# Kernel tuning notes

Measured on AMD Instinct MI355X. Metric: run time of the kernel, lower is better.

The kernel has to match this reference:

```python
import jax, jax.numpy as jnp
import numpy as np
import math

H = 12          # num_attention_heads
DIM = 768       # hidden_size
HD = DIM // H   # attention_head_size
B = 8           # batch
S = 1024        # max_seqlen
NNZ = B * S     # total_nnz (all sequences full length)


def setup_inputs() -> dict:
    key = jax.random.key(0)
    k1, k2, k3, k4 = jax.random.split(key, 4)
    hidden_states = jax.random.normal(k1, (NNZ, DIM), jnp.float32)
    cu_seqlens = jnp.arange(B + 1, dtype=jnp.int32) * S
    indices = jnp.arange(NNZ, dtype=jnp.int32)
    attn_mask = jnp.ones((B, S), jnp.int32)
    bias = jax.random.normal(k2, (B, H, S, S), jnp.float32) * 0.1
    slopes = jax.random.uniform(k3, (H,), jnp.float32)
    # Wqkv = nn.Linear(DIM, 3*DIM): weight (3*DIM, DIM), bias (3*DIM,)
    Wqkv_w = jax.random.normal(k4, (3 * DIM, DIM), jnp.float32) * (1.0 / math.sqrt(DIM))
    Wqkv_b = jnp.zeros((3 * DIM,), jnp.float32)
    return {
        "hidden_states": hidden_states,
        "cu_seqlens": cu_seqlens,
        "max_seqlen": S,
        "indices": indices,
        "attn_mask": attn_mask,
        "bias": bias,
        "slopes": slopes,
        "Wqkv_w": Wqkv_w,
        "Wqkv_b": Wqkv_b,
    }


def reference(hidden_states, cu_seqlens, max_seqlen, indices, attn_mask, bias, slopes, Wqkv_w, Wqkv_b):
    nnz, dim = hidden_states.shape
    batch = cu_seqlens.shape[0] - 1
    hd = dim // H
    # fused QKV projection on unpadded tokens
    qkv = hidden_states @ Wqkv_w.T + Wqkv_b                      # (nnz, 3*dim)
    # pad_input: scatter tokens into dense (batch*seqlen, 3*dim)
    padded = jnp.zeros((batch * max_seqlen, 3 * dim), qkv.dtype).at[indices].set(qkv)
    qkv = padded.reshape(batch, max_seqlen, 3, H, hd)            # (b, s, 3, h, d)
    q, k, v = qkv[:, :, 0], qkv[:, :, 1], qkv[:, :, 2]           # (b, s, h, d)
    scores = jnp.einsum('bqhd,bkhd->bhqk', q, k) / math.sqrt(hd) + bias
    probs = jax.nn.softmax(scores, axis=-1)                      # (b, h, q, k)
    attn = jnp.einsum('bhqk,bkhd->bqhd', probs, v)               # (b, s, h, d)
    # unpad_input_only: gather valid tokens (attn_mask selects same positions as indices)
    flat = attn.reshape(batch * max_seqlen, dim)
    return flat[indices].reshape(nnz, dim)
```

## Files before the change

### kernel.cpp

```cpp
#include <hip/hip_runtime.h>

#define H_      12
#define DIM_    768
#define HD_     64
#define BATCH_  8
#define SEQ_    1024
#define NNZ_    8192
#define N3_     2304

typedef short sh8 __attribute__((ext_vector_type(8)));
typedef float f32x4 __attribute__((ext_vector_type(4)));

__device__ __forceinline__ unsigned short f2bf(float f) {
    unsigned u = __float_as_uint(f);
    u += 0x7fff + ((u >> 16) & 1);
    return (unsigned short)(u >> 16);
}

__device__ __forceinline__ void glds16(const unsigned short* g, unsigned short* l) {
    __builtin_amdgcn_global_load_lds(
        (const __attribute__((address_space(1))) unsigned int*)g,
        (__attribute__((address_space(3))) unsigned int*)l, 16, 0, 0);
}

__global__ void prep(const float* __restrict__ hidden,
                     const float* __restrict__ W,
                     const int* __restrict__ indices,
                     unsigned short* __restrict__ Xbf,
                     unsigned short* __restrict__ Wbf,
                     int* __restrict__ inv) {
    const int XN4 = NNZ_ * DIM_ / 4;
    const int WN4 = N3_ * DIM_ / 4;
    int i = blockIdx.x * blockDim.x + threadIdx.x;
    if (i < XN4) {
        float4 f = ((const float4*)hidden)[i];
        ushort4 u;
        u.x = f2bf(f.x); u.y = f2bf(f.y); u.z = f2bf(f.z); u.w = f2bf(f.w);
        ((ushort4*)Xbf)[i] = u;
    } else if (i < XN4 + WN4) {
        int k = i - XN4;
        float4 f = ((const float4*)W)[k];
        ushort4 u;
        u.x = f2bf(f.x); u.y = f2bf(f.y); u.z = f2bf(f.z); u.w = f2bf(f.w);
        ((ushort4*)Wbf)[k] = u;
    }
    if (i < NNZ_) inv[indices[i]] = i;
}

#define BK 32
__launch_bounds__(256)
__global__ void qkv_gemm(const unsigned short* __restrict__ X,
                         const unsigned short* __restrict__ W,
                         const float* __restrict__ bqkv,
                         const int* __restrict__ indices,
                         unsigned short* __restrict__ qkvbf) {
    __shared__ __align__(16) unsigned short As[128 * BK];
    __shared__ __align__(16) unsigned short Bs[128 * BK];

    const int bm = blockIdx.x * 128;
    const int bn = blockIdx.y * 128;
    const int t = threadIdx.x;
    const int wave = t >> 6;
    const int lane = t & 63;
    const int l16 = lane & 15;
    const int quad = lane >> 4;
    const int wm = (wave & 1) * 64;
    const int wn = (wave >> 1) * 64;

    f32x4 acc[4][4];
    for (int i = 0; i < 4; i++)
        for (int j = 0; j < 4; j++)
            for (int r = 0; r < 4; r++) acc[i][j][r] = 0.f;

    const int c0 = wave * 2;
    const int r0 = c0 * 16 + (lane >> 2);
    const int colA = (lane & 3) * 8;
    const unsigned short* gA0 = &X[(size_t)(bm + r0) * DIM_ + colA];
    const unsigned short* gA1 = &X[(size_t)(bm + r0 + 16) * DIM_ + colA];
    const unsigned short* gB0 = &W[(size_t)(bn + r0) * DIM_ + colA];
    const unsigned short* gB1 = &W[(size_t)(bn + r0 + 16) * DIM_ + colA];
    unsigned short* lA0 = &As[c0 * 512];
    unsigned short* lA1 = &As[c0 * 512 + 512];
    unsigned short* lB0 = &Bs[c0 * 512];
    unsigned short* lB1 = &Bs[c0 * 512 + 512];

    for (int kk = 0; kk < DIM_; kk += BK) {
        __syncthreads();
        glds16(gA0 + kk, lA0);
        glds16(gA1 + kk, lA1);
        glds16(gB0 + kk, lB0);
        glds16(gB1 + kk, lB1);
        __syncthreads();

        sh8 af[4], wf[4];
        for (int i = 0; i < 4; i++)
            af[i] = *(const sh8*)&As[(wm + i * 16 + l16) * BK + quad * 8];
        for (int j = 0; j < 4; j++)
            wf[j] = *(const sh8*)&Bs[(wn + j * 16 + l16) * BK + quad * 8];
        for (int i = 0; i < 4; i++)
            for (int j = 0; j < 4; j++)
                acc[i][j] = __builtin_amdgcn_mfma_f32_16x16x32_bf16(af[i], wf[j], acc[i][j], 0, 0, 0);
    }

    const size_t plane = (size_t)BATCH_ * H_ * SEQ_ * HD_;
    for (int i = 0; i < 4; i++) {
        for (int r = 0; r < 4; r++) {
            int m = bm + wm + i * 16 + quad * 4 + r;
            int pos = indices[m];
            int b = pos >> 10;
            int s = pos & 1023;
            for (int j = 0; j < 4; j++) {
                int n = bn + wn + j * 16 + l16;
                float val = acc[i][j][r] + bqkv[n];
                int which = n / DIM_;
                int nn = n - which * DIM_;
                int hh = nn >> 6;
                int d = nn & 63;
                size_t off;
                if (which == 2)
                    off = 2 * plane + (((size_t)b * H_ + hh) * HD_ + d) * SEQ_ + s;
                else
                    off = (size_t)which * plane + (((size_t)b * H_ + hh) * SEQ_ + s) * HD_ + d;
                qkvbf[off] = f2bf(val);
            }
        }
    }
}

#define LDP 72
__launch_bounds__(256)
__global__ void attn(const unsigned short* __restrict__ qkvbf,
                     const float* __restrict__ bias,
                     const int* __restrict__ inv,
                     float* __restrict__ out) {
    __shared__ __align__(16) unsigned short Ks2[2][64 * 32];
    __shared__ __align__(16) unsigned short Vt2[2][64 * 32];
    __shared__ __align__(16) unsigned short Ps[4][16 * LDP];

    const int qt = blockIdx.x;
    const int bh = blockIdx.y;
    const int t = threadIdx.x;
    const int wave = t >> 6;
    const int lane = t & 63;
    const int l16 = lane & 15;
    const int quad = lane >> 4;

    const size_t plane = (size_t)BATCH_ * H_ * SEQ_ * HD_;
    const unsigned short* Q  = qkvbf + (size_t)bh * SEQ_ * HD_;
    const unsigned short* K  = Q + plane;
    const unsigned short* Vt = qkvbf + 2 * plane + (size_t)bh * HD_ * SEQ_;

    const int q0 = qt * 64 + wave * 16;

    sh8 aq[2];
    for (int kk2 = 0; kk2 < 2; kk2++)
        aq[kk2] = *(const sh8*)&Q[(size_t)(q0 + l16) * HD_ + kk2 * 32 + quad * 8];

    float l_p[4] = {0.f, 0.f, 0.f, 0.f};
    f32x4 o[4];
    for (int j = 0; j < 4; j++)
        for (int r = 0; r < 4; r++) o[j][r] = 0.f;

    const float scale = 0.125f;
    const float* brow = bias + (size_t)bh * SEQ_ * SEQ_;

    const int lrow = wave * 16 + (lane >> 2);
    const int lcol = (lane & 3) * 8;
    const unsigned short* gK = &K[(size_t)lrow * HD_ + lcol];
    const unsigned short* gV = &Vt[(size_t)lrow * SEQ_ + lcol];
    unsigned short* lK0 = &Ks2[0][wave * 512];
    unsigned short* lK1 = &Ks2[1][wave * 512];
    unsigned short* lV0 = &Vt2[0][wave * 512];
    unsigned short* lV1 = &Vt2[1][wave * 512];

    for (int kt = 0; kt < 16; kt++) {
        const int k0 = kt * 64;

        float bv[4][4];
        for (int j = 0; j < 4; j++)
            for (int r = 0; r < 4; r++)
                bv[j][r] = brow[(size_t)(q0 + quad * 4 + r) * SEQ_ + k0 + j * 16 + l16];

        __syncthreads();
        glds16(gK + (size_t)k0 * HD_,      lK0);
        glds16(gK + (size_t)k0 * HD_ + 32, lK1);
        glds16(gV + k0,      lV0);
        glds16(gV + k0 + 32, lV1);
        __syncthreads();

        f32x4 sc[4];
        for (int j = 0; j < 4; j++)
            for (int r = 0; r < 4; r++) sc[j][r] = 0.f;
        for (int kk2 = 0; kk2 < 2; kk2++)
            for (int j = 0; j < 4; j++) {
                sh8 bk = *(const sh8*)&Ks2[kk2][(j * 16 + l16) * 32 + quad * 8];
                sc[j] = __builtin_amdgcn_mfma_f32_16x16x32_bf16(aq[kk2], bk, sc[j], 0, 0, 0);
            }

        for (int j = 0; j < 4; j++)
            for (int r = 0; r < 4; r++) {
                float p = __expf(sc[j][r] * scale + bv[j][r]);
                l_p[r] += p;
                Ps[wave][(quad * 4 + r) * LDP + j * 16 + l16] = f2bf(p);
            }

        for (int kk2 = 0; kk2 < 2; kk2++) {
            sh8 ap = *(const sh8*)&Ps[wave][l16 * LDP + kk2 * 32 + quad * 8];
            for (int j = 0; j < 4; j++) {
                sh8 vv = *(const sh8*)&Vt2[kk2][(j * 16 + l16) * 32 + quad * 8];
                o[j] = __builtin_amdgcn_mfma_f32_16x16x32_bf16(ap, vv, o[j], 0, 0, 0);
            }
        }
    }

    float l_i[4];
    for (int r = 0; r < 4; r++) {
        float s0 = l_p[r];
        for (int off = 1; off < 16; off <<= 1)
            s0 += __shfl_xor(s0, off, 64);
        l_i[r] = s0;
    }

    const int b = bh / H_;
    const int hh = bh % H_;
    for (int r = 0; r < 4; r++) {
        int srow_q = q0 + quad * 4 + r;
        int pos = b * SEQ_ + srow_q;
        int i_out = inv[pos];
        float rl = 1.0f / l_i[r];
        for (int j = 0; j < 4; j++)
            out[(size_t)i_out * DIM_ + hh * HD_ + j * 16 + l16] = o[j][r] * rl;
    }
}

extern "C" void kernel_launch(void* const* d_in, const int* in_sizes, int n_in,
                              void* d_out, int out_size, void* d_ws, size_t ws_size,
                              hipStream_t stream) {
    const float* hidden  = (const float*)d_in[0];
    const int*   indices = (const int*)d_in[3];
    const float* bias    = (const float*)d_in[5];
    const float* Wqkv_w  = (const float*)d_in[7];
    const float* Wqkv_b  = (const float*)d_in[8];
    float* out = (float*)d_out;

    char* ws = (char*)d_ws;
    unsigned short* Xbf   = (unsigned short*)ws;
    unsigned short* Wbf   = (unsigned short*)(ws + 12582912);
    unsigned short* qkvbf = (unsigned short*)(ws + 16121856);
    int* inv              = (int*)(ws + 53870592);

    const int XN4 = NNZ_ * DIM_ / 4;
    const int WN4 = N3_ * DIM_ / 4;
    prep<<<(XN4 + WN4 + 255) / 256, 256, 0, stream>>>(hidden, Wqkv_w, indices, Xbf, Wbf, inv);
    qkv_gemm<<<dim3(NNZ_ / 128, N3_ / 128), 256, 0, stream>>>(Xbf, Wbf, Wqkv_b, indices, qkvbf);
    attn<<<dim3(SEQ_ / 64, BATCH_ * H_), 256, 0, stream>>>(qkvbf, bias, inv, out);
}
```

Measured before the change: 639.4 us.

## Double-buffer K/V tiles, prefetch bias, swizzle LDS and transpose score MFMA

Rewrites the attention kernel's main loop to double-buffer the K and V tiles in LDS, issuing the next tile's async loads before computing on the current one and dropping one barrier per iteration. Bias is prefetched one tile ahead as float4 rows, made possible by swapping the MFMA operands so each lane holds contiguous key columns. An XOR swizzle on LDS slots is meant to reduce bank conflicts, and the block index is remapped to improve cache locality. It also sets an occupancy hint of 3 blocks per SM. Costs are a larger LDS footprint and more register pressure, which could limit occupancy.

```diff
diff --git a/kernel.cpp b/kernel.cpp
--- a/kernel.cpp
+++ b/kernel.cpp
@@ -128,22 +128,26 @@
 }
 
 #define LDP 72
-__launch_bounds__(256)
+__launch_bounds__(256, 3)
 __global__ void attn(const unsigned short* __restrict__ qkvbf,
                      const float* __restrict__ bias,
                      const int* __restrict__ inv,
                      float* __restrict__ out) {
-    __shared__ __align__(16) unsigned short Ks2[2][64 * 32];
-    __shared__ __align__(16) unsigned short Vt2[2][64 * 32];
+    __shared__ __align__(16) unsigned short Kp[2][2][64 * 32];
+    __shared__ __align__(16) unsigned short Vp[2][2][64 * 32];
     __shared__ __align__(16) unsigned short Ps[4][16 * LDP];
 
-    const int qt = blockIdx.x;
-    const int bh = blockIdx.y;
+    const int orig = blockIdx.y * gridDim.x + blockIdx.x;
+    const int swz = (orig & 7) * 192 + (orig >> 3);
+    const int qt = swz & 15;
+    const int bh = swz >> 4;
+
     const int t = threadIdx.x;
     const int wave = t >> 6;
     const int lane = t & 63;
     const int l16 = lane & 15;
     const int quad = lane >> 4;
+    const int qx = quad ^ (l16 & 3);
 
     const size_t plane = (size_t)BATCH_ * H_ * SEQ_ * HD_;
     const unsigned short* Q  = qkvbf + (size_t)bh * SEQ_ * HD_;
@@ -156,70 +160,96 @@
     for (int kk2 = 0; kk2 < 2; kk2++)
         aq[kk2] = *(const sh8*)&Q[(size_t)(q0 + l16) * HD_ + kk2 * 32 + quad * 8];
 
-    float l_p[4] = {0.f, 0.f, 0.f, 0.f};
+    float lsum = 0.f;
     f32x4 o[4];
     for (int j = 0; j < 4; j++)
         for (int r = 0; r < 4; r++) o[j][r] = 0.f;
 
     const float scale = 0.125f;
-    const float* brow = bias + (size_t)bh * SEQ_ * SEQ_;
+    const float* brow4 = bias + (size_t)bh * SEQ_ * SEQ_ + (size_t)(q0 + l16) * SEQ_ + quad * 4;
 
     const int lrow = wave * 16 + (lane >> 2);
-    const int lcol = (lane & 3) * 8;
-    const unsigned short* gK = &K[(size_t)lrow * HD_ + lcol];
-    const unsigned short* gV = &Vt[(size_t)lrow * SEQ_ + lcol];
-    unsigned short* lK0 = &Ks2[0][wave * 512];
-    unsigned short* lK1 = &Ks2[1][wave * 512];
-    unsigned short* lV0 = &Vt2[0][wave * 512];
-    unsigned short* lV1 = &Vt2[1][wave * 512];
+    const int lslot = (lane & 3) ^ ((lane >> 2) & 3);
+    const unsigned short* gK = &K[(size_t)lrow * HD_ + lslot * 8];
+    const unsigned short* gV = &Vt[(size_t)lrow * SEQ_ + lslot * 8];
+    unsigned short* lK0[2] = { &Kp[0][0][wave * 512], &Kp[0][1][wave * 512] };
+    unsigned short* lK1[2] = { &Kp[1][0][wave * 512], &Kp[1][1][wave * 512] };
+    unsigned short* lV0[2] = { &Vp[0][0][wave * 512], &Vp[0][1][wave * 512] };
+    unsigned short* lV1[2] = { &Vp[1][0][wave * 512], &Vp[1][1][wave * 512] };
+
+    glds16(gK,      lK0[0]);
+    glds16(gK + 32, lK0[1]);
+    glds16(gV,      lV0[0]);
+    glds16(gV + 32, lV0[1]);
+    float4 bv4[4];
+    for (int j = 0; j < 4; j++)
+        bv4[j] = *(const float4*)(brow4 + j * 16);
+    __syncthreads();
 
     for (int kt = 0; kt < 16; kt++) {
-        const int k0 = kt * 64;
-
-        float bv[4][4];
-        for (int j = 0; j < 4; j++)
-            for (int r = 0; r < 4; r++)
-                bv[j][r] = brow[(size_t)(q0 + quad * 4 + r) * SEQ_ + k0 + j * 16 + l16];
-
-        __syncthreads();
-        glds16(gK + (size_t)k0 * HD_,      lK0);
-        glds16(gK + (size_t)k0 * HD_ + 32, lK1);
-        glds16(gV + k0,      lV0);
-        glds16(gV + k0 + 32, lV1);
-        __syncthreads();
+        const int cur = kt & 1;
+
+        if (kt < 15) {
+            const int k0n = (kt + 1) * 64;
+            if (cur == 0) {
+                glds16(gK + (size_t)k0n * HD_,      lK1[0]);
+                glds16(gK + (size_t)k0n * HD_ + 32, lK1[1]);
+                glds16(gV + k0n,      lV1[0]);
+                glds16(gV + k0n + 32, lV1[1]);
+            } else {
+                glds16(gK + (size_t)k0n * HD_,      lK0[0]);
+                glds16(gK + (size_t)k0n * HD_ + 32, lK0[1]);
+                glds16(gV + k0n,      lV0[0]);
+                glds16(gV + k0n + 32, lV0[1]);
+            }
+        }
+        float4 bvn[4];
+        {
+            const int kb = ((kt + 1) & 15) * 64;
+            for (int j = 0; j < 4; j++)
+                bvn[j] = *(const float4*)(brow4 + kb + j * 16);
+        }
+        __builtin_amdgcn_sched_barrier(0);
 
         f32x4 sc[4];
         for (int j = 0; j < 4; j++)
             for (int r = 0; r < 4; r++) sc[j][r] = 0.f;
         for (int kk2 = 0; kk2 < 2; kk2++)
             for (int j = 0; j < 4; j++) {
-                sh8 bk = *(const sh8*)&Ks2[kk2][(j * 16 + l16) * 32 + quad * 8];
-                sc[j] = __builtin_amdgcn_mfma_f32_16x16x32_bf16(aq[kk2], bk, sc[j], 0, 0, 0);
-            }
-
-        for (int j = 0; j < 4; j++)
-            for (int r = 0; r < 4; r++) {
-                float p = __expf(sc[j][r] * scale + bv[j][r]);
-                l_p[r] += p;
-                Ps[wave][(quad * 4 + r) * LDP + j * 16 + l16] = f2bf(p);
-            }
+                sh8 bk = *(const sh8*)&Kp[cur][kk2][(j * 16 + l16) * 32 + qx * 8];
+                sc[j] = __builtin_amdgcn_mfma_f32_16x16x32_bf16(bk, aq[kk2], sc[j], 0, 0, 0);
+            }
+
+        for (int j = 0; j < 4; j++) {
+            float4 bb = bv4[j];
+            float p0 = __expf(sc[j][0] * scale + bb.x);
+            float p1 = __expf(sc[j][1] * scale + bb.y);
+            float p2 = __expf(sc[j][2] * scale + bb.z);
+            float p3 = __expf(sc[j][3] * scale + bb.w);
+            lsum += (p0 + p1) + (p2 + p3);
+            ushort4 u;
+            u.x = f2bf(p0); u.y = f2bf(p1); u.z = f2bf(p2); u.w = f2bf(p3);
+            *(ushort4*)&Ps[wave][l16 * LDP + j * 16 + quad * 4] = u;
+        }
 
         for (int kk2 = 0; kk2 < 2; kk2++) {
             sh8 ap = *(const sh8*)&Ps[wave][l16 * LDP + kk2 * 32 + quad * 8];
             for (int j = 0; j < 4; j++) {
-                sh8 vv = *(const sh8*)&Vt2[kk2][(j * 16 + l16) * 32 + quad * 8];
-                o[j] = __builtin_amdgcn_mfma_f32_16x16x32_bf16(ap, vv, o[j], 0, 0, 0);
-            }
-        }
-    }
-
-    float l_i[4];
-    for (int r = 0; r < 4; r++) {
-        float s0 = l_p[r];
-        for (int off = 1; off < 16; off <<= 1)
-            s0 += __shfl_xor(s0, off, 64);
-        l_i[r] = s0;
-    }
+                sh8 vvf = *(const sh8*)&Vp[cur][kk2][(j * 16 + l16) * 32 + qx * 8];
+                o[j] = __builtin_amdgcn_mfma_f32_16x16x32_bf16(ap, vvf, o[j], 0, 0, 0);
+            }
+        }
+
+        __syncthreads();
+        for (int j = 0; j < 4; j++) bv4[j] = bvn[j];
+    }
+
+    float s0 = lsum;
+    s0 += __shfl_xor(s0, 16, 64);
+    s0 += __shfl_xor(s0, 32, 64);
+    float rl[4];
+    for (int r = 0; r < 4; r++)
+        rl[r] = 1.0f / __shfl(s0, quad * 4 + r, 64);
 
     const int b = bh / H_;
     const int hh = bh % H_;
@@ -227,9 +257,8 @@
         int srow_q = q0 + quad * 4 + r;
         int pos = b * SEQ_ + srow_q;
         int i_out = inv[pos];
-        float rl = 1.0f / l_i[r];
-        for (int j = 0; j < 4; j++)
-            out[(size_t)i_out * DIM_ + hh * HD_ + j * 16 + l16] = o[j][r] * rl;
+        for (int j = 0; j < 4; j++)
+            out[(size_t)i_out * DIM_ + hh * HD_ + j * 16 + l16] = o[j][r] * rl[r];
     }
 }
 
```

Result: faster. 624.9 us (-2.3%).
